# Kernel optimization log

Hardware: AMD Instinct MI355X
Metric: run time of the kernel (lower is better)

Reference implementation:

```python
import jax, jax.numpy as jnp
import numpy as np

N = 100_000      # nodes
E = 1_200_000    # edges (before self-loops)
F_IN = 128       # num_node_features
G = 256          # number of graphs in the batch
C = 10           # num_classes
NEG_SLOPE = 0.2  # PyG GATConv default


def setup_inputs() -> dict:
    key = jax.random.key(0)
    ks = jax.random.split(key, 20)
    x = jax.random.normal(ks[0], (N, F_IN), jnp.float32)
    edge_index = jax.random.randint(ks[1], (2, E), 0, N, dtype=jnp.int32)
    # sorted graph assignment covering all G graphs (no empty segments)
    batch = (jnp.arange(N, dtype=jnp.int32) * G) // N

    def lin(k, fi, fo):
        return jax.random.normal(k, (fi, fo), jnp.float32) * (1.0 / np.sqrt(fi))

    dims = [(F_IN, 16), (16, 32), (32, 64)]
    params = {}
    for i, (fi, fo) in enumerate(dims, start=1):
        params[f"W{i}"] = lin(ks[3 * i], fi, fo)
        params[f"a{i}_src"] = jax.random.normal(ks[3 * i + 1], (fo,), jnp.float32) * 0.1
        params[f"a{i}_dst"] = jax.random.normal(ks[3 * i + 2], (fo,), jnp.float32) * 0.1
        params[f"b{i}"] = jnp.zeros((fo,), jnp.float32)
    params["fc_w"] = lin(ks[15], 64, C)
    params["fc_b"] = jnp.zeros((C,), jnp.float32)
    return {"x": x, "edge_index": edge_index, "batch": batch, **params}


def _gat_layer(x, src, dst, W, a_src, a_dst, b):
    # h = Theta x; e_ij = LeakyReLU(a_src.h_j + a_dst.h_i), softmax over dst i
    h = x @ W                                     # [N, F]
    s = h @ a_src                                 # [N]
    d = h @ a_dst                                 # [N]
    logits = jax.nn.leaky_relu(s[src] + d[dst], NEG_SLOPE)   # [E+N]
    m = jax.ops.segment_max(logits, dst, num_segments=N)     # per-dst max
    ex = jnp.exp(logits - m[dst])
    denom = jax.ops.segment_sum(ex, dst, num_segments=N)
    alpha = ex / (denom[dst] + 1e-16)             # [E+N]
    out = jax.ops.segment_sum(alpha[:, None] * h[src], dst, num_segments=N)
    return out + b


def reference(x, edge_index, batch, W1, a1_src, a1_dst, b1, W2, a2_src, a2_dst, b2,
              W3, a3_src, a3_dst, b3, fc_w, fc_b):
    # add self-loops (PyG GATConv default) -> every dst segment non-empty
    loops = jnp.arange(N, dtype=edge_index.dtype)
    src = jnp.concatenate([edge_index[0], loops])
    dst = jnp.concatenate([edge_index[1], loops])

    h = jax.nn.relu(_gat_layer(x, src, dst, W1, a1_src, a1_dst, b1))
    # F.dropout(training=False) is a no-op in eval
    h = jax.nn.relu(_gat_layer(h, src, dst, W2, a2_src, a2_dst, b2))
    h = jax.nn.relu(_gat_layer(h, src, dst, W3, a3_src, a3_dst, b3))
    pooled = jax.ops.segment_max(h, batch, num_segments=G)   # global_max_pool [G, 64]
    logits = pooled @ fc_w + fc_b
    return jax.nn.log_softmax(logits, axis=1)
```

## Files before the change

kernel.cpp:

```cpp
#include <hip/hip_runtime.h>
#include <hip/hip_bf16.h>
#include <hip/hip_fp16.h>
#include <math.h>

#define NEG_SLOPE 0.2f
#define NCHUNK 1024
#define BSHIFT 9
#define BNODES 512

__device__ __forceinline__ float leaky(float x) { return x > 0.f ? x : NEG_SLOPE * x; }
__device__ __forceinline__ int usan(int v, int n) { return ((unsigned)v < (unsigned)n) ? v : 0; }

__global__ void chunk_hist(const int* __restrict__ dst, int E, int Ec, int nbuck,
                           int* __restrict__ hmatT) {
    extern __shared__ int hist[];
    int c = blockIdx.x;
    for (int b = threadIdx.x; b < nbuck; b += 256) hist[b] = 0;
    __syncthreads();
    int lo = c * Ec, hi = min(E, lo + Ec);
    for (int e = lo + threadIdx.x; e < hi; e += 256) atomicAdd(&hist[dst[e] >> BSHIFT], 1);
    __syncthreads();
    for (int b = threadIdx.x; b < nbuck; b += 256) hmatT[b * NCHUNK + c] = hist[b];
}

__global__ void mat_scan(int* __restrict__ hmatT, int* __restrict__ btot) {
    __shared__ int wsum[4];
    int b = blockIdx.x;
    int t = threadIdx.x;
    int lane = t & 63, wave = t >> 6;
    int base = b * NCHUNK + t * 4;
    int a0 = hmatT[base], a1 = hmatT[base + 1], a2 = hmatT[base + 2], a3 = hmatT[base + 3];
    int ts = a0 + a1 + a2 + a3;
    int incl = ts;
#pragma unroll
    for (int o = 1; o < 64; o <<= 1) {
        int v = __shfl_up(incl, o);
        if (lane >= o) incl += v;
    }
    if (lane == 63) wsum[wave] = incl;
    __syncthreads();
    int wadd = 0;
#pragma unroll
    for (int w = 0; w < 4; w++) if (w < wave) wadd += wsum[w];
    int excl = wadd + incl - ts;
    hmatT[base] = excl;
    hmatT[base + 1] = excl + a0;
    hmatT[base + 2] = excl + a0 + a1;
    hmatT[base + 3] = excl + a0 + a1 + a2;
    if (t == 255) btot[b] = wadd + incl;
}

__global__ void base_scan(const int* __restrict__ btot, int nbuck, int* __restrict__ bbase,
                          int* __restrict__ offs, int N, int E) {
    __shared__ int tsum[256];
    int t = threadIdx.x;
    int v = (t < nbuck) ? btot[t] : 0;
    tsum[t] = v;
    __syncthreads();
    for (int o = 1; o < 256; o <<= 1) {
        int add = (t >= o) ? tsum[t - o] : 0;
        __syncthreads();
        tsum[t] += add;
        __syncthreads();
    }
    if (t <= nbuck) bbase[t] = (t == 0) ? 0 : tsum[t - 1];
    if (t == 0) offs[N] = N + E;
}

__global__ void chunk_scatter(const int* __restrict__ src, const int* __restrict__ dst,
                              int E, int Ec, int nbuck, const int* __restrict__ hmatT,
                              const int* __restrict__ bbase, int* __restrict__ bbuf) {
    extern __shared__ int cur[];
    int c = blockIdx.x;
    for (int b = threadIdx.x; b < nbuck; b += 256) cur[b] = bbase[b] + hmatT[b * NCHUNK + c];
    __syncthreads();
    int lo = c * Ec, hi = min(E, lo + Ec);
    for (int e = lo + threadIdx.x; e < hi; e += 256) {
        int d = dst[e];
        int b = d >> BSHIFT;
        int p = atomicAdd(&cur[b], 1);
        bbuf[p] = (src[e] << BSHIFT) | (d & (BNODES - 1));
    }
}

__global__ void bucket_build(const int* __restrict__ bbase, const int* __restrict__ bbuf,
                             int N, int* __restrict__ offs, int* __restrict__ csr) {
    __shared__ int hist[BNODES];
    __shared__ int offl[BNODES];
    __shared__ int cur[BNODES];
    int b = blockIdx.x;
    int t = threadIdx.x;
    hist[t] = 0;
    __syncthreads();
    int lo = bbase[b], hi = bbase[b + 1];
    for (int j = lo + t; j < hi; j += BNODES) atomicAdd(&hist[bbuf[j] & (BNODES - 1)], 1);
    __syncthreads();
    int own = hist[t];
    for (int o = 1; o < BNODES; o <<= 1) {
        int add = (t >= o) ? hist[t - o] : 0;
        __syncthreads();
        hist[t] += add;
        __syncthreads();
    }
    int excl = hist[t] - own;
    int n = (b << BSHIFT) + t;
    int off_n = n + bbase[b] + excl;
    offl[t] = off_n;
    cur[t] = 0;
    if (n < N) {
        offs[n] = off_n;
        csr[off_n] = n;
    }
    __syncthreads();
    for (int j = lo + t; j < hi; j += BNODES) {
        int v = bbuf[j];
        int ld = v & (BNODES - 1);
        int r = atomicAdd(&cur[ld], 1);
        csr[offl[ld] + 1 + r] = v >> BSHIFT;
    }
}


template <int FIN, int FOUT>
__global__ void transform(const float* __restrict__ xin, const float* __restrict__ W,
                          const float* __restrict__ adst,
                          __half* __restrict__ h, float* __restrict__ dv, int N) {
    constexpr int TPN = FOUT / 4;
    constexpr int BN  = 256 / TPN;
    constexpr int PITCH = FIN + 4;
    __shared__ float xs[BN * PITCH];
    __shared__ float wl[FIN * FOUT];
    __shared__ float bl[FOUT];
    for (int j = threadIdx.x; j < FIN * FOUT; j += 256) wl[j] = W[j];
    if (threadIdx.x < FOUT) bl[threadIdx.x] = adst[threadIdx.x];
    int base = blockIdx.x * BN;
    constexpr int NV = BN * FIN / 4;
    const float4* xg = (const float4*)xin + (size_t)base * (FIN / 4);
    int limv = ((N - base) * FIN) >> 2;
    for (int v = threadIdx.x; v < NV; v += 256) {
        int n = v / (FIN / 4), c = v % (FIN / 4);
        float4 val = (v < limv) ? xg[v] : make_float4(0.f, 0.f, 0.f, 0.f);
        *(float4*)&xs[n * PITCH + c * 4] = val;
    }
    __syncthreads();
    int node_l = threadIdx.x / TPN;
    int fq = (threadIdx.x % TPN) * 4;
    int node = base + node_l;
    const float* xrow = &xs[node_l * PITCH];
    float4 acc = make_float4(0.f, 0.f, 0.f, 0.f);
#pragma unroll 8
    for (int k = 0; k < FIN; k++) {
        float xv = xrow[k];
        float4 w4 = *(const float4*)&wl[k * FOUT + fq];
        acc.x += xv * w4.x; acc.y += xv * w4.y; acc.z += xv * w4.z; acc.w += xv * w4.w;
    }
    if (node < N) {
        __half2* hp = (__half2*)(h + (size_t)node * FOUT + fq);
        hp[0] = __floats2half2_rn(acc.x, acc.y);
        hp[1] = __floats2half2_rn(acc.z, acc.w);
        float dp = acc.x * bl[fq] + acc.y * bl[fq + 1] + acc.z * bl[fq + 2] + acc.w * bl[fq + 3];
#pragma unroll
        for (int o = TPN / 2; o > 0; o >>= 1) dp += __shfl_xor(dp, o);
        if (fq == 0) dv[node] = dp;
    }
}


template <int FI, int FO>
__global__ void gat_trans(const __half* __restrict__ h, const float* __restrict__ asrc,
                          const float* __restrict__ dv, const int* __restrict__ offs,
                          const int* __restrict__ csr, const float* __restrict__ bias,
                          const float* __restrict__ Wn, const float* __restrict__ an_d,
                          __half* __restrict__ h2, float* __restrict__ dv2, int N) {
    constexpr int L  = FI / 8;
    constexpr int L2 = 2 * L;
    constexpr int CPL = FO / L2;
    constexpr int NPB = 256 / L2;
    __shared__ float wl[FI * FO];
    __shared__ float bl[FO];
    for (int j = threadIdx.x; j < FI * FO; j += 256) wl[j] = Wn[j];
    if (threadIdx.x < FO) bl[threadIdx.x] = an_d[threadIdx.x];
    __syncthreads();
    int lane  = threadIdx.x % L;
    int lane2 = threadIdx.x % L2;
    int wlane = threadIdx.x & 63;
    int half  = (threadIdx.x / L) & 1;
    int grpbase = wlane & ~(L2 - 1);
    int i = blockIdx.x * NPB + threadIdx.x / L2;
    if (i >= N) return;
    float asr[8];
#pragma unroll
    for (int k = 0; k < 8; k++) asr[k] = asrc[lane * 8 + k];
    int beg = offs[i], end = offs[i + 1];
    float di = dv[i];
    float acc[8];
#pragma unroll
    for (int c = 0; c < 8; c++) acc[c] = 0.f;
    float ssum = 0.f;

    int j0 = beg + 4 * half;
    int j1 = j0 + 8;
    bool vA = (j0 + 4 <= end);
    bool vB = (j1 + 4 <= end);
    int j0e = vA ? j0 : beg;
    int a0 = usan(csr[j0e], N),     a1 = usan(csr[j0e + 1], N);
    int a2 = usan(csr[j0e + 2], N), a3 = usan(csr[j0e + 3], N);
    uint4 uA0 = *((const uint4*)(h + (size_t)a0 * FI) + lane);
    uint4 uA1 = *((const uint4*)(h + (size_t)a1 * FI) + lane);
    uint4 uA2 = *((const uint4*)(h + (size_t)a2 * FI) + lane);
    uint4 uA3 = *((const uint4*)(h + (size_t)a3 * FI) + lane);
    int j1e = vB ? j1 : beg;
    int b0 = usan(csr[j1e], N),     b1 = usan(csr[j1e + 1], N);
    int b2 = usan(csr[j1e + 2], N), b3 = usan(csr[j1e + 3], N);
    while (vA) {
        int j2 = j1 + 8;
        bool vC = vB && (j2 + 4 <= end);
        uint4 uB0 = *((const uint4*)(h + (size_t)b0 * FI) + lane);
        uint4 uB1 = *((const uint4*)(h + (size_t)b1 * FI) + lane);
        uint4 uB2 = *((const uint4*)(h + (size_t)b2 * FI) + lane);
        uint4 uB3 = *((const uint4*)(h + (size_t)b3 * FI) + lane);
        int j2e = vC ? j2 : beg;
        int c0 = usan(csr[j2e], N),     c1 = usan(csr[j2e + 1], N);
        int c2 = usan(csr[j2e + 2], N), c3 = usan(csr[j2e + 3], N);
        float2 f0[4], f1[4], f2[4], f3[4];
#pragma unroll
        for (int c = 0; c < 4; c++) {
            f0[c] = __half22float2(((const __half2*)&uA0)[c]);
            f1[c] = __half22float2(((const __half2*)&uA1)[c]);
            f2[c] = __half22float2(((const __half2*)&uA2)[c]);
            f3[c] = __half22float2(((const __half2*)&uA3)[c]);
        }
        float p0 = 0.f, p1 = 0.f, p2 = 0.f, p3 = 0.f;
#pragma unroll
        for (int c = 0; c < 4; c++) {
            p0 += f0[c].x * asr[2 * c] + f0[c].y * asr[2 * c + 1];
            p1 += f1[c].x * asr[2 * c] + f1[c].y * asr[2 * c + 1];
            p2 += f2[c].x * asr[2 * c] + f2[c].y * asr[2 * c + 1];
            p3 += f3[c].x * asr[2 * c] + f3[c].y * asr[2 * c + 1];
        }
#pragma unroll
        for (int o = 1; o < L; o <<= 1) {
            p0 += __shfl_xor(p0, o); p1 += __shfl_xor(p1, o);
            p2 += __shfl_xor(p2, o); p3 += __shfl_xor(p3, o);
        }
        float w0 = __expf(leaky(p0 + di));
        float w1 = __expf(leaky(p1 + di));
        float w2 = __expf(leaky(p2 + di));
        float w3 = __expf(leaky(p3 + di));
        ssum += (w0 + w1) + (w2 + w3);
#pragma unroll
        for (int c = 0; c < 4; c++) {
            acc[2 * c]     += w0 * f0[c].x + w1 * f1[c].x + w2 * f2[c].x + w3 * f3[c].x;
            acc[2 * c + 1] += w0 * f0[c].y + w1 * f1[c].y + w2 * f2[c].y + w3 * f3[c].y;
        }
        uA0 = uB0; uA1 = uB1; uA2 = uB2; uA3 = uB3;
        b0 = c0; b1 = c1; b2 = c2; b3 = c3;
        j0 = j1; j1 = j2; vA = vB; vB = vC;
    }
    int rem = end - j0;
    if (rem > 0) {
        int o1 = rem > 1 ? 1 : 0;
        int o2 = rem > 2 ? 2 : o1;
        int t0 = usan(csr[j0], N), t1 = usan(csr[j0 + o1], N), t2 = usan(csr[j0 + o2], N);
        uint4 r0 = *((const uint4*)(h + (size_t)t0 * FI) + lane);
        uint4 r1 = *((const uint4*)(h + (size_t)t1 * FI) + lane);
        uint4 r2 = *((const uint4*)(h + (size_t)t2 * FI) + lane);
        float2 g0[4], g1[4], g2[4];
#pragma unroll
        for (int c = 0; c < 4; c++) {
            g0[c] = __half22float2(((const __half2*)&r0)[c]);
            g1[c] = __half22float2(((const __half2*)&r1)[c]);
            g2[c] = __half22float2(((const __half2*)&r2)[c]);
        }
        float q0 = 0.f, q1 = 0.f, q2 = 0.f;
#pragma unroll
        for (int c = 0; c < 4; c++) {
            q0 += g0[c].x * asr[2 * c] + g0[c].y * asr[2 * c + 1];
            q1 += g1[c].x * asr[2 * c] + g1[c].y * asr[2 * c + 1];
            q2 += g2[c].x * asr[2 * c] + g2[c].y * asr[2 * c + 1];
        }
#pragma unroll
        for (int o = 1; o < L; o <<= 1) {
            q0 += __shfl_xor(q0, o); q1 += __shfl_xor(q1, o); q2 += __shfl_xor(q2, o);
        }
        float w0t = __expf(leaky(q0 + di));
        float w1t = rem > 1 ? __expf(leaky(q1 + di)) : 0.f;
        float w2t = rem > 2 ? __expf(leaky(q2 + di)) : 0.f;
        ssum += w0t + w1t + w2t;
#pragma unroll
        for (int c = 0; c < 4; c++) {
            acc[2 * c]     += w0t * g0[c].x + w1t * g1[c].x + w2t * g2[c].x;
            acc[2 * c + 1] += w0t * g0[c].y + w1t * g1[c].y + w2t * g2[c].y;
        }
    }
#pragma unroll
    for (int c = 0; c < 8; c++) acc[c] += __shfl_xor(acc[c], L);
    ssum += __shfl_xor(ssum, L);

    float inv = 1.0f / ssum;
    float4 ba = ((const float4*)bias)[lane * 2];
    float4 bb = ((const float4*)bias)[lane * 2 + 1];
    float yv[8];
    yv[0] = fmaxf(acc[0] * inv + ba.x, 0.f);
    yv[1] = fmaxf(acc[1] * inv + ba.y, 0.f);
    yv[2] = fmaxf(acc[2] * inv + ba.z, 0.f);
    yv[3] = fmaxf(acc[3] * inv + ba.w, 0.f);
    yv[4] = fmaxf(acc[4] * inv + bb.x, 0.f);
    yv[5] = fmaxf(acc[5] * inv + bb.y, 0.f);
    yv[6] = fmaxf(acc[6] * inv + bb.z, 0.f);
    yv[7] = fmaxf(acc[7] * inv + bb.w, 0.f);
    int colbase = lane2 * CPL;
    float oacc[CPL];
#pragma unroll
    for (int c = 0; c < CPL; c++) oacc[c] = 0.f;
#pragma unroll
    for (int jj = 0; jj < L; jj++) {
        float v[8];
#pragma unroll
        for (int r = 0; r < 8; r++) v[r] = __shfl(yv[r], grpbase + jj);
#pragma unroll
        for (int r = 0; r < 8; r++) {
            const float* wrow = &wl[(jj * 8 + r) * FO + colbase];
#pragma unroll
            for (int c = 0; c < CPL; c++) oacc[c] += v[r] * wrow[c];
        }
    }
    __half2 hp[CPL / 2];
#pragma unroll
    for (int c = 0; c < CPL / 2; c++) hp[c] = __floats2half2_rn(oacc[2 * c], oacc[2 * c + 1]);
    *((uint4*)(h2 + (size_t)i * FO + colbase)) = *(uint4*)&hp[0];
    float dp = 0.f;
#pragma unroll
    for (int c = 0; c < CPL; c++) dp += oacc[c] * bl[colbase + c];
#pragma unroll
    for (int o = 1; o < L2; o <<= 1) dp += __shfl_xor(dp, o);
    if (lane2 == 0) dv2[i] = dp;
}


template <int F>
__global__ void gat_fused(const __half* __restrict__ h, const float* __restrict__ asrc,
                          const float* __restrict__ dv, const int* __restrict__ offs,
                          const int* __restrict__ csr, const float* __restrict__ bias,
                          __half* __restrict__ y, int N) {
    constexpr int L  = F / 8;
    constexpr int L2 = 2 * L;
    constexpr int NPB = 256 / L2;
    int lane  = threadIdx.x % L;
    int half  = (threadIdx.x / L) & 1;
    int i = blockIdx.x * NPB + threadIdx.x / L2;
    if (i >= N) return;
    float asr[8];
#pragma unroll
    for (int k = 0; k < 8; k++) asr[k] = asrc[lane * 8 + k];
    int beg = offs[i], end = offs[i + 1];
    float di = dv[i];
    float acc[8];
#pragma unroll
    for (int c = 0; c < 8; c++) acc[c] = 0.f;
    float ssum = 0.f;

    int j0 = beg + 4 * half;
    int j1 = j0 + 8;
    bool vA = (j0 + 4 <= end);
    bool vB = (j1 + 4 <= end);
    int j0e = vA ? j0 : beg;
    int a0 = usan(csr[j0e], N),     a1 = usan(csr[j0e + 1], N);
    int a2 = usan(csr[j0e + 2], N), a3 = usan(csr[j0e + 3], N);
    uint4 uA0 = *((const uint4*)(h + (size_t)a0 * F) + lane);
    uint4 uA1 = *((const uint4*)(h + (size_t)a1 * F) + lane);
    uint4 uA2 = *((const uint4*)(h + (size_t)a2 * F) + lane);
    uint4 uA3 = *((const uint4*)(h + (size_t)a3 * F) + lane);
    int j1e = vB ? j1 : beg;
    int b0 = usan(csr[j1e], N),     b1 = usan(csr[j1e + 1], N);
    int b2 = usan(csr[j1e + 2], N), b3 = usan(csr[j1e + 3], N);
    while (vA) {
        int j2 = j1 + 8;
        bool vC = vB && (j2 + 4 <= end);
        uint4 uB0 = *((const uint4*)(h + (size_t)b0 * F) + lane);
        uint4 uB1 = *((const uint4*)(h + (size_t)b1 * F) + lane);
        uint4 uB2 = *((const uint4*)(h + (size_t)b2 * F) + lane);
        uint4 uB3 = *((const uint4*)(h + (size_t)b3 * F) + lane);
        int j2e = vC ? j2 : beg;
        int c0 = usan(csr[j2e], N),     c1 = usan(csr[j2e + 1], N);
        int c2 = usan(csr[j2e + 2], N), c3 = usan(csr[j2e + 3], N);
        float2 f0[4], f1[4], f2[4], f3[4];
#pragma unroll
        for (int c = 0; c < 4; c++) {
            f0[c] = __half22float2(((const __half2*)&uA0)[c]);
            f1[c] = __half22float2(((const __half2*)&uA1)[c]);
            f2[c] = __half22float2(((const __half2*)&uA2)[c]);
            f3[c] = __half22float2(((const __half2*)&uA3)[c]);
        }
        float p0 = 0.f, p1 = 0.f, p2 = 0.f, p3 = 0.f;
#pragma unroll
        for (int c = 0; c < 4; c++) {
            p0 += f0[c].x * asr[2 * c] + f0[c].y * asr[2 * c + 1];
            p1 += f1[c].x * asr[2 * c] + f1[c].y * asr[2 * c + 1];
            p2 += f2[c].x * asr[2 * c] + f2[c].y * asr[2 * c + 1];
            p3 += f3[c].x * asr[2 * c] + f3[c].y * asr[2 * c + 1];
        }
#pragma unroll
        for (int o = 1; o < L; o <<= 1) {
            p0 += __shfl_xor(p0, o); p1 += __shfl_xor(p1, o);
            p2 += __shfl_xor(p2, o); p3 += __shfl_xor(p3, o);
        }
        float w0 = __expf(leaky(p0 + di));
        float w1 = __expf(leaky(p1 + di));
        float w2 = __expf(leaky(p2 + di));
        float w3 = __expf(leaky(p3 + di));
        ssum += (w0 + w1) + (w2 + w3);
#pragma unroll
        for (int c = 0; c < 4; c++) {
            acc[2 * c]     += w0 * f0[c].x + w1 * f1[c].x + w2 * f2[c].x + w3 * f3[c].x;
            acc[2 * c + 1] += w0 * f0[c].y + w1 * f1[c].y + w2 * f2[c].y + w3 * f3[c].y;
        }
        uA0 = uB0; uA1 = uB1; uA2 = uB2; uA3 = uB3;
        b0 = c0; b1 = c1; b2 = c2; b3 = c3;
        j0 = j1; j1 = j2; vA = vB; vB = vC;
    }
    int rem = end - j0;
    if (rem > 0) {
        int o1 = rem > 1 ? 1 : 0;
        int o2 = rem > 2 ? 2 : o1;
        int t0 = usan(csr[j0], N), t1 = usan(csr[j0 + o1], N), t2 = usan(csr[j0 + o2], N);
        uint4 r0 = *((const uint4*)(h + (size_t)t0 * F) + lane);
        uint4 r1 = *((const uint4*)(h + (size_t)t1 * F) + lane);
        uint4 r2 = *((const uint4*)(h + (size_t)t2 * F) + lane);
        float2 g0[4], g1[4], g2[4];
#pragma unroll
        for (int c = 0; c < 4; c++) {
            g0[c] = __half22float2(((const __half2*)&r0)[c]);
            g1[c] = __half22float2(((const __half2*)&r1)[c]);
            g2[c] = __half22float2(((const __half2*)&r2)[c]);
        }
        float q0 = 0.f, q1 = 0.f, q2 = 0.f;
#pragma unroll
        for (int c = 0; c < 4; c++) {
            q0 += g0[c].x * asr[2 * c] + g0[c].y * asr[2 * c + 1];
            q1 += g1[c].x * asr[2 * c] + g1[c].y * asr[2 * c + 1];
            q2 += g2[c].x * asr[2 * c] + g2[c].y * asr[2 * c + 1];
        }
#pragma unroll
        for (int o = 1; o < L; o <<= 1) {
            q0 += __shfl_xor(q0, o); q1 += __shfl_xor(q1, o); q2 += __shfl_xor(q2, o);
        }
        float w0t = __expf(leaky(q0 + di));
        float w1t = rem > 1 ? __expf(leaky(q1 + di)) : 0.f;
        float w2t = rem > 2 ? __expf(leaky(q2 + di)) : 0.f;
        ssum += w0t + w1t + w2t;
#pragma unroll
        for (int c = 0; c < 4; c++) {
            acc[2 * c]     += w0t * g0[c].x + w1t * g1[c].x + w2t * g2[c].x;
            acc[2 * c + 1] += w0t * g0[c].y + w1t * g1[c].y + w2t * g2[c].y;
        }
    }
#pragma unroll
    for (int c = 0; c < 8; c++) acc[c] += __shfl_xor(acc[c], L);
    ssum += __shfl_xor(ssum, L);
    if (half == 0) {
        float inv = 1.0f / ssum;
        float4 ba = ((const float4*)bias)[lane * 2];
        float4 bb = ((const float4*)bias)[lane * 2 + 1];
        __half2 o[4];
        o[0] = __floats2half2_rn(fmaxf(acc[0] * inv + ba.x, 0.f), fmaxf(acc[1] * inv + ba.y, 0.f));
        o[1] = __floats2half2_rn(fmaxf(acc[2] * inv + ba.z, 0.f), fmaxf(acc[3] * inv + ba.w, 0.f));
        o[2] = __floats2half2_rn(fmaxf(acc[4] * inv + bb.x, 0.f), fmaxf(acc[5] * inv + bb.y, 0.f));
        o[3] = __floats2half2_rn(fmaxf(acc[6] * inv + bb.z, 0.f), fmaxf(acc[7] * inv + bb.w, 0.f));
        ((uint4*)(y + (size_t)i * F))[lane] = *(uint4*)&o[0];
    }
}


__global__ void pool_head(const __half* __restrict__ y, const float* __restrict__ fcw,
                          const float* __restrict__ fcb, float* __restrict__ out,
                          int N, int G, int C) {
    __shared__ float red[256];
    __shared__ float pl[64];
    int g = blockIdx.x;
    long long gl = g;
    int start = (int)((gl * N + G - 1) / G);
    int end = (int)(((gl + 1) * N + G - 1) / G);
    int f = threadIdx.x & 63, w = threadIdx.x >> 6;
    float m = 0.f;
    for (int i = start + w; i < end; i += 4) m = fmaxf(m, __half2float(y[(size_t)i * 64 + f]));
    red[threadIdx.x] = m;
    __syncthreads();
    if (threadIdx.x < 64) {
        pl[f] = fmaxf(fmaxf(red[f], red[64 + f]), fmaxf(red[128 + f], red[192 + f]));
    }
    __syncthreads();
    if (threadIdx.x < 64) {
        int c = threadIdx.x;
        float z = -1e30f;
        if (c < C) {
            z = fcb[c];
            for (int k = 0; k < 64; k++) z += pl[k] * fcw[k * 10 + c];
        }
        float zm = z;
#pragma unroll
        for (int o = 1; o < 16; o <<= 1) zm = fmaxf(zm, __shfl_xor(zm, o));
        float e = (c < C) ? __expf(z - zm) : 0.f;
        float se = e;
#pragma unroll
        for (int o = 1; o < 16; o <<= 1) se += __shfl_xor(se, o);
        if (c < C) out[g * C + c] = z - zm - logf(se);
    }
}


extern "C" void kernel_launch(void* const* d_in, const int* in_sizes, int n_in,
                              void* d_out, int out_size, void* d_ws, size_t ws_size,
                              hipStream_t stream) {
    const float* x    = (const float*)d_in[0];
    const int*   eidx = (const int*)d_in[1];
    const float* W1 = (const float*)d_in[3];
    const float* a1s = (const float*)d_in[4];
    const float* a1d = (const float*)d_in[5];
    const float* b1 = (const float*)d_in[6];
    const float* W2 = (const float*)d_in[7];
    const float* a2s = (const float*)d_in[8];
    const float* a2d = (const float*)d_in[9];
    const float* b2 = (const float*)d_in[10];
    const float* W3 = (const float*)d_in[11];
    const float* a3s = (const float*)d_in[12];
    const float* a3d = (const float*)d_in[13];
    const float* b3 = (const float*)d_in[14];
    const float* fcw = (const float*)d_in[15];
    const float* fcb = (const float*)d_in[16];
    float* out = (float*)d_out;

    const int N = in_sizes[2];
    const int E = in_sizes[1] / 2;
    const int C = in_sizes[16];
    const int G = out_size / C;

    const int* src = eidx;
    const int* dst = eidx + E;

    size_t off = 0;
    auto alloc = [&](size_t bytes) -> void* {
        void* p = (char*)d_ws + off;
        off += (bytes + 255) & ~(size_t)255;
        return p;
    };
    int* offs   = (int*)alloc((size_t)(N + 1) * 4);
    int* csr    = (int*)alloc((size_t)(E + N) * 4 + 256);
    float* dbufA = (float*)alloc((size_t)N * 4);
    float* dbufB = (float*)alloc((size_t)N * 4);
    __half* hA = (__half*)alloc((size_t)N * 64 * 2);
    __half* hB = (__half*)alloc((size_t)N * 64 * 2);

    const int NBUCK = (N + BNODES - 1) >> BSHIFT;
    const int Ec = (E + NCHUNK - 1) / NCHUNK;
    int* hmatT = (int*)alloc((size_t)NBUCK * NCHUNK * 4);
    int* btot  = (int*)alloc((size_t)NBUCK * 4);
    int* bbase = (int*)alloc((size_t)(NBUCK + 1) * 4);
    int* bbuf  = (int*)hB;

    const size_t histBytes = (size_t)NBUCK * 4;

    chunk_hist<<<NCHUNK, 256, histBytes, stream>>>(dst, E, Ec, NBUCK, hmatT);
    mat_scan<<<NBUCK, 256, 0, stream>>>(hmatT, btot);
    base_scan<<<1, 256, 0, stream>>>(btot, NBUCK, bbase, offs, N, E);
    chunk_scatter<<<NCHUNK, 256, histBytes, stream>>>(src, dst, E, Ec, NBUCK, hmatT, bbase, bbuf);
    bucket_build<<<NBUCK, BNODES, 0, stream>>>(bbase, bbuf, N, offs, csr);

    transform<128, 16><<<(N + 63) / 64, 256, 0, stream>>>(x, W1, a1d, hA, dbufA, N);
    gat_trans<16, 32><<<(N + 63) / 64, 256, 0, stream>>>(hA, a1s, dbufA, offs, csr, b1,
                                                         W2, a2d, hB, dbufB, N);
    gat_trans<32, 64><<<(N + 31) / 32, 256, 0, stream>>>(hB, a2s, dbufB, offs, csr, b2,
                                                         W3, a3d, hA, dbufA, N);
    gat_fused<64><<<(N + 15) / 16, 256, 0, stream>>>(hA, a3s, dbufA, offs, csr, b3, hB, N);

    pool_head<<<G, 256, 0, stream>>>(hB, fcw, fcb, out, N, G, C);
}
```

Measured before the change: 274.5 us.

## Fuse global max pool into last GAT layer via atomicMax; shrink CSR buckets

The last GAT layer now max-pools its ReLU outputs straight into a per-graph pooled buffer. It does this with atomicMax on the float bits, going through a shared-memory reduction when a block covers a single graph. This removes the write and reread of the final N×64 half activations and leaves a tiny head kernel. The CSR bucket size also drops from 512 to 256 nodes, and the block-level scans in base_scan and bucket_build switch to wave-shuffle scans with 512 threads. The risk is that NBUCK (about 391) must stay at or below 512 threads, and the pooled buffer must be zeroed each call, which base_scan now does.

```diff
diff --git a/kernel.cpp b/kernel.cpp
--- a/kernel.cpp
+++ b/kernel.cpp
@@ -5,8 +5,8 @@
 
 #define NEG_SLOPE 0.2f
 #define NCHUNK 1024
-#define BSHIFT 9
-#define BNODES 512
+#define BSHIFT 8
+#define BNODES 256
 
 __device__ __forceinline__ float leaky(float x) { return x > 0.f ? x : NEG_SLOPE * x; }
 __device__ __forceinline__ int usan(int v, int n) { return ((unsigned)v < (unsigned)n) ? v : 0; }
@@ -51,20 +51,27 @@
 }
 
 __global__ void base_scan(const int* __restrict__ btot, int nbuck, int* __restrict__ bbase,
-                          int* __restrict__ offs, int N, int E) {
-    __shared__ int tsum[256];
+                          int* __restrict__ offs, int N, int E, float* __restrict__ pooled,
+                          int PG) {
+    __shared__ int wsum[8];
     int t = threadIdx.x;
+    int lane = t & 63, wave = t >> 6;
     int v = (t < nbuck) ? btot[t] : 0;
-    tsum[t] = v;
-    __syncthreads();
-    for (int o = 1; o < 256; o <<= 1) {
-        int add = (t >= o) ? tsum[t - o] : 0;
-        __syncthreads();
-        tsum[t] += add;
-        __syncthreads();
-    }
-    if (t <= nbuck) bbase[t] = (t == 0) ? 0 : tsum[t - 1];
+    int incl = v;
+#pragma unroll
+    for (int o = 1; o < 64; o <<= 1) {
+        int s = __shfl_up(incl, o);
+        if (lane >= o) incl += s;
+    }
+    if (lane == 63) wsum[wave] = incl;
+    __syncthreads();
+    int wadd = 0;
+#pragma unroll
+    for (int w = 0; w < 8; w++) if (w < wave) wadd += wsum[w];
+    incl += wadd;
+    if (t <= nbuck) bbase[t] = incl - v;
     if (t == 0) offs[N] = N + E;
+    for (int k = t; k < PG; k += 512) pooled[k] = 0.f;
 }
 
 __global__ void chunk_scatter(const int* __restrict__ src, const int* __restrict__ dst,
@@ -88,21 +95,28 @@
     __shared__ int hist[BNODES];
     __shared__ int offl[BNODES];
     __shared__ int cur[BNODES];
+    __shared__ int wsum[4];
     int b = blockIdx.x;
     int t = threadIdx.x;
+    int lane = t & 63, wave = t >> 6;
     hist[t] = 0;
     __syncthreads();
     int lo = bbase[b], hi = bbase[b + 1];
     for (int j = lo + t; j < hi; j += BNODES) atomicAdd(&hist[bbuf[j] & (BNODES - 1)], 1);
     __syncthreads();
     int own = hist[t];
-    for (int o = 1; o < BNODES; o <<= 1) {
-        int add = (t >= o) ? hist[t - o] : 0;
-        __syncthreads();
-        hist[t] += add;
-        __syncthreads();
-    }
-    int excl = hist[t] - own;
+    int incl = own;
+#pragma unroll
+    for (int o = 1; o < 64; o <<= 1) {
+        int s = __shfl_up(incl, o);
+        if (lane >= o) incl += s;
+    }
+    if (lane == 63) wsum[wave] = incl;
+    __syncthreads();
+    int wadd = 0;
+#pragma unroll
+    for (int w = 0; w < 4; w++) if (w < wave) wadd += wsum[w];
+    int excl = wadd + incl - own;
     int n = (b << BSHIFT) + t;
     int off_n = n + bbase[b] + excl;
     offl[t] = off_n;
@@ -342,170 +356,184 @@
 __global__ void gat_fused(const __half* __restrict__ h, const float* __restrict__ asrc,
                           const float* __restrict__ dv, const int* __restrict__ offs,
                           const int* __restrict__ csr, const float* __restrict__ bias,
-                          __half* __restrict__ y, int N) {
+                          float* __restrict__ pooled, int Gn, int N) {
     constexpr int L  = F / 8;
     constexpr int L2 = 2 * L;
     constexpr int NPB = 256 / L2;
+    __shared__ unsigned pl[64];
     int lane  = threadIdx.x % L;
     int half  = (threadIdx.x / L) & 1;
     int i = blockIdx.x * NPB + threadIdx.x / L2;
-    if (i >= N) return;
-    float asr[8];
-#pragma unroll
-    for (int k = 0; k < 8; k++) asr[k] = asrc[lane * 8 + k];
-    int beg = offs[i], end = offs[i + 1];
-    float di = dv[i];
-    float acc[8];
-#pragma unroll
-    for (int c = 0; c < 8; c++) acc[c] = 0.f;
-    float ssum = 0.f;
-
-    int j0 = beg + 4 * half;
-    int j1 = j0 + 8;
-    bool vA = (j0 + 4 <= end);
-    bool vB = (j1 + 4 <= end);
-    int j0e = vA ? j0 : beg;
-    int a0 = usan(csr[j0e], N),     a1 = usan(csr[j0e + 1], N);
-    int a2 = usan(csr[j0e + 2], N), a3 = usan(csr[j0e + 3], N);
-    uint4 uA0 = *((const uint4*)(h + (size_t)a0 * F) + lane);
-    uint4 uA1 = *((const uint4*)(h + (size_t)a1 * F) + lane);
-    uint4 uA2 = *((const uint4*)(h + (size_t)a2 * F) + lane);
-    uint4 uA3 = *((const uint4*)(h + (size_t)a3 * F) + lane);
-    int j1e = vB ? j1 : beg;
-    int b0 = usan(csr[j1e], N),     b1 = usan(csr[j1e + 1], N);
-    int b2 = usan(csr[j1e + 2], N), b3 = usan(csr[j1e + 3], N);
-    while (vA) {
-        int j2 = j1 + 8;
-        bool vC = vB && (j2 + 4 <= end);
-        uint4 uB0 = *((const uint4*)(h + (size_t)b0 * F) + lane);
-        uint4 uB1 = *((const uint4*)(h + (size_t)b1 * F) + lane);
-        uint4 uB2 = *((const uint4*)(h + (size_t)b2 * F) + lane);
-        uint4 uB3 = *((const uint4*)(h + (size_t)b3 * F) + lane);
-        int j2e = vC ? j2 : beg;
-        int c0 = usan(csr[j2e], N),     c1 = usan(csr[j2e + 1], N);
-        int c2 = usan(csr[j2e + 2], N), c3 = usan(csr[j2e + 3], N);
-        float2 f0[4], f1[4], f2[4], f3[4];
-#pragma unroll
-        for (int c = 0; c < 4; c++) {
-            f0[c] = __half22float2(((const __half2*)&uA0)[c]);
-            f1[c] = __half22float2(((const __half2*)&uA1)[c]);
-            f2[c] = __half22float2(((const __half2*)&uA2)[c]);
-            f3[c] = __half22float2(((const __half2*)&uA3)[c]);
-        }
-        float p0 = 0.f, p1 = 0.f, p2 = 0.f, p3 = 0.f;
-#pragma unroll
-        for (int c = 0; c < 4; c++) {
-            p0 += f0[c].x * asr[2 * c] + f0[c].y * asr[2 * c + 1];
-            p1 += f1[c].x * asr[2 * c] + f1[c].y * asr[2 * c + 1];
-            p2 += f2[c].x * asr[2 * c] + f2[c].y * asr[2 * c + 1];
-            p3 += f3[c].x * asr[2 * c] + f3[c].y * asr[2 * c + 1];
-        }
-#pragma unroll
-        for (int o = 1; o < L; o <<= 1) {
-            p0 += __shfl_xor(p0, o); p1 += __shfl_xor(p1, o);
-            p2 += __shfl_xor(p2, o); p3 += __shfl_xor(p3, o);
-        }
-        float w0 = __expf(leaky(p0 + di));
-        float w1 = __expf(leaky(p1 + di));
-        float w2 = __expf(leaky(p2 + di));
-        float w3 = __expf(leaky(p3 + di));
-        ssum += (w0 + w1) + (w2 + w3);
-#pragma unroll
-        for (int c = 0; c < 4; c++) {
-            acc[2 * c]     += w0 * f0[c].x + w1 * f1[c].x + w2 * f2[c].x + w3 * f3[c].x;
-            acc[2 * c + 1] += w0 * f0[c].y + w1 * f1[c].y + w2 * f2[c].y + w3 * f3[c].y;
-        }
-        uA0 = uB0; uA1 = uB1; uA2 = uB2; uA3 = uB3;
-        b0 = c0; b1 = c1; b2 = c2; b3 = c3;
-        j0 = j1; j1 = j2; vA = vB; vB = vC;
-    }
-    int rem = end - j0;
-    if (rem > 0) {
-        int o1 = rem > 1 ? 1 : 0;
-        int o2 = rem > 2 ? 2 : o1;
-        int t0 = usan(csr[j0], N), t1 = usan(csr[j0 + o1], N), t2 = usan(csr[j0 + o2], N);
-        uint4 r0 = *((const uint4*)(h + (size_t)t0 * F) + lane);
-        uint4 r1 = *((const uint4*)(h + (size_t)t1 * F) + lane);
-        uint4 r2 = *((const uint4*)(h + (size_t)t2 * F) + lane);
-        float2 g0[4], g1[4], g2[4];
-#pragma unroll
-        for (int c = 0; c < 4; c++) {
-            g0[c] = __half22float2(((const __half2*)&r0)[c]);
-            g1[c] = __half22float2(((const __half2*)&r1)[c]);
-            g2[c] = __half22float2(((const __half2*)&r2)[c]);
-        }
-        float q0 = 0.f, q1 = 0.f, q2 = 0.f;
-#pragma unroll
-        for (int c = 0; c < 4; c++) {
-            q0 += g0[c].x * asr[2 * c] + g0[c].y * asr[2 * c + 1];
-            q1 += g1[c].x * asr[2 * c] + g1[c].y * asr[2 * c + 1];
-            q2 += g2[c].x * asr[2 * c] + g2[c].y * asr[2 * c + 1];
-        }
-#pragma unroll
-        for (int o = 1; o < L; o <<= 1) {
-            q0 += __shfl_xor(q0, o); q1 += __shfl_xor(q1, o); q2 += __shfl_xor(q2, o);
-        }
-        float w0t = __expf(leaky(q0 + di));
-        float w1t = rem > 1 ? __expf(leaky(q1 + di)) : 0.f;
-        float w2t = rem > 2 ? __expf(leaky(q2 + di)) : 0.f;
-        ssum += w0t + w1t + w2t;
-#pragma unroll
-        for (int c = 0; c < 4; c++) {
-            acc[2 * c]     += w0t * g0[c].x + w1t * g1[c].x + w2t * g2[c].x;
-            acc[2 * c + 1] += w0t * g0[c].y + w1t * g1[c].y + w2t * g2[c].y;
-        }
-    }
-#pragma unroll
-    for (int c = 0; c < 8; c++) acc[c] += __shfl_xor(acc[c], L);
-    ssum += __shfl_xor(ssum, L);
-    if (half == 0) {
+    bool active = (i < N);
+    float yf[8];
+#pragma unroll
+    for (int c = 0; c < 8; c++) yf[c] = 0.f;
+    if (active) {
+        float asr[8];
+#pragma unroll
+        for (int k = 0; k < 8; k++) asr[k] = asrc[lane * 8 + k];
+        int beg = offs[i], end = offs[i + 1];
+        float di = dv[i];
+        float acc[8];
+#pragma unroll
+        for (int c = 0; c < 8; c++) acc[c] = 0.f;
+        float ssum = 0.f;
+
+        int j0 = beg + 4 * half;
+        int j1 = j0 + 8;
+        bool vA = (j0 + 4 <= end);
+        bool vB = (j1 + 4 <= end);
+        int j0e = vA ? j0 : beg;
+        int a0 = usan(csr[j0e], N),     a1 = usan(csr[j0e + 1], N);
+        int a2 = usan(csr[j0e + 2], N), a3 = usan(csr[j0e + 3], N);
+        uint4 uA0 = *((const uint4*)(h + (size_t)a0 * F) + lane);
+        uint4 uA1 = *((const uint4*)(h + (size_t)a1 * F) + lane);
+        uint4 uA2 = *((const uint4*)(h + (size_t)a2 * F) + lane);
+        uint4 uA3 = *((const uint4*)(h + (size_t)a3 * F) + lane);
+        int j1e = vB ? j1 : beg;
+        int b0 = usan(csr[j1e], N),     b1 = usan(csr[j1e + 1], N);
+        int b2 = usan(csr[j1e + 2], N), b3 = usan(csr[j1e + 3], N);
+        while (vA) {
+            int j2 = j1 + 8;
+            bool vC = vB && (j2 + 4 <= end);
+            uint4 uB0 = *((const uint4*)(h + (size_t)b0 * F) + lane);
+            uint4 uB1 = *((const uint4*)(h + (size_t)b1 * F) + lane);
+            uint4 uB2 = *((const uint4*)(h + (size_t)b2 * F) + lane);
+            uint4 uB3 = *((const uint4*)(h + (size_t)b3 * F) + lane);
+            int j2e = vC ? j2 : beg;
+            int c0 = usan(csr[j2e], N),     c1 = usan(csr[j2e + 1], N);
+            int c2 = usan(csr[j2e + 2], N), c3 = usan(csr[j2e + 3], N);
+            float2 f0[4], f1[4], f2[4], f3[4];
+#pragma unroll
+            for (int c = 0; c < 4; c++) {
+                f0[c] = __half22float2(((const __half2*)&uA0)[c]);
+                f1[c] = __half22float2(((const __half2*)&uA1)[c]);
+                f2[c] = __half22float2(((const __half2*)&uA2)[c]);
+                f3[c] = __half22float2(((const __half2*)&uA3)[c]);
+            }
+            float p0 = 0.f, p1 = 0.f, p2 = 0.f, p3 = 0.f;
+#pragma unroll
+            for (int c = 0; c < 4; c++) {
+                p0 += f0[c].x * asr[2 * c] + f0[c].y * asr[2 * c + 1];
+                p1 += f1[c].x * asr[2 * c] + f1[c].y * asr[2 * c + 1];
+                p2 += f2[c].x * asr[2 * c] + f2[c].y * asr[2 * c + 1];
+                p3 += f3[c].x * asr[2 * c] + f3[c].y * asr[2 * c + 1];
+            }
+#pragma unroll
+            for (int o = 1; o < L; o <<= 1) {
+                p0 += __shfl_xor(p0, o); p1 += __shfl_xor(p1, o);
+                p2 += __shfl_xor(p2, o); p3 += __shfl_xor(p3, o);
+            }
+            float w0 = __expf(leaky(p0 + di));
+            float w1 = __expf(leaky(p1 + di));
+            float w2 = __expf(leaky(p2 + di));
+            float w3 = __expf(leaky(p3 + di));
+            ssum += (w0 + w1) + (w2 + w3);
+#pragma unroll
+            for (int c = 0; c < 4; c++) {
+                acc[2 * c]     += w0 * f0[c].x + w1 * f1[c].x + w2 * f2[c].x + w3 * f3[c].x;
+                acc[2 * c + 1] += w0 * f0[c].y + w1 * f1[c].y + w2 * f2[c].y + w3 * f3[c].y;
+            }
+            uA0 = uB0; uA1 = uB1; uA2 = uB2; uA3 = uB3;
+            b0 = c0; b1 = c1; b2 = c2; b3 = c3;
+            j0 = j1; j1 = j2; vA = vB; vB = vC;
+        }
+        int rem = end - j0;
+        if (rem > 0) {
+            int o1 = rem > 1 ? 1 : 0;
+            int o2 = rem > 2 ? 2 : o1;
+            int t0 = usan(csr[j0], N), t1 = usan(csr[j0 + o1], N), t2 = usan(csr[j0 + o2], N);
+            uint4 r0 = *((const uint4*)(h + (size_t)t0 * F) + lane);
+            uint4 r1 = *((const uint4*)(h + (size_t)t1 * F) + lane);
+            uint4 r2 = *((const uint4*)(h + (size_t)t2 * F) + lane);
+            float2 g0[4], g1[4], g2[4];
+#pragma unroll
+            for (int c = 0; c < 4; c++) {
+                g0[c] = __half22float2(((const __half2*)&r0)[c]);
+                g1[c] = __half22float2(((const __half2*)&r1)[c]);
+                g2[c] = __half22float2(((const __half2*)&r2)[c]);
+            }
+            float q0 = 0.f, q1 = 0.f, q2 = 0.f;
+#pragma unroll
+            for (int c = 0; c < 4; c++) {
+                q0 += g0[c].x * asr[2 * c] + g0[c].y * asr[2 * c + 1];
+                q1 += g1[c].x * asr[2 * c] + g1[c].y * asr[2 * c + 1];
+                q2 += g2[c].x * asr[2 * c] + g2[c].y * asr[2 * c + 1];
+            }
+#pragma unroll
+            for (int o = 1; o < L; o <<= 1) {
+                q0 += __shfl_xor(q0, o); q1 += __shfl_xor(q1, o); q2 += __shfl_xor(q2, o);
+            }
+            float w0t = __expf(leaky(q0 + di));
+            float w1t = rem > 1 ? __expf(leaky(q1 + di)) : 0.f;
+            float w2t = rem > 2 ? __expf(leaky(q2 + di)) : 0.f;
+            ssum += w0t + w1t + w2t;
+#pragma unroll
+            for (int c = 0; c < 4; c++) {
+                acc[2 * c]     += w0t * g0[c].x + w1t * g1[c].x + w2t * g2[c].x;
+                acc[2 * c + 1] += w0t * g0[c].y + w1t * g1[c].y + w2t * g2[c].y;
+            }
+        }
+#pragma unroll
+        for (int c = 0; c < 8; c++) acc[c] += __shfl_xor(acc[c], L);
+        ssum += __shfl_xor(ssum, L);
         float inv = 1.0f / ssum;
         float4 ba = ((const float4*)bias)[lane * 2];
         float4 bb = ((const float4*)bias)[lane * 2 + 1];
-        __half2 o[4];
-        o[0] = __floats2half2_rn(fmaxf(acc[0] * inv + ba.x, 0.f), fmaxf(acc[1] * inv + ba.y, 0.f));
-        o[1] = __floats2half2_rn(fmaxf(acc[2] * inv + ba.z, 0.f), fmaxf(acc[3] * inv + ba.w, 0.f));
-        o[2] = __floats2half2_rn(fmaxf(acc[4] * inv + bb.x, 0.f), fmaxf(acc[5] * inv + bb.y, 0.f));
-        o[3] = __floats2half2_rn(fmaxf(acc[6] * inv + bb.z, 0.f), fmaxf(acc[7] * inv + bb.w, 0.f));
-        ((uint4*)(y + (size_t)i * F))[lane] = *(uint4*)&o[0];
-    }
-}
-
-
-__global__ void pool_head(const __half* __restrict__ y, const float* __restrict__ fcw,
-                          const float* __restrict__ fcb, float* __restrict__ out,
-                          int N, int G, int C) {
-    __shared__ float red[256];
+        yf[0] = fmaxf(acc[0] * inv + ba.x, 0.f);
+        yf[1] = fmaxf(acc[1] * inv + ba.y, 0.f);
+        yf[2] = fmaxf(acc[2] * inv + ba.z, 0.f);
+        yf[3] = fmaxf(acc[3] * inv + ba.w, 0.f);
+        yf[4] = fmaxf(acc[4] * inv + bb.x, 0.f);
+        yf[5] = fmaxf(acc[5] * inv + bb.y, 0.f);
+        yf[6] = fmaxf(acc[6] * inv + bb.z, 0.f);
+        yf[7] = fmaxf(acc[7] * inv + bb.w, 0.f);
+    }
+    int i0 = blockIdx.x * NPB;
+    int ilast = min(i0 + NPB, N) - 1;
+    int gfirst = (int)(((long long)i0 * Gn) / N);
+    int glast  = (int)(((long long)ilast * Gn) / N);
+    if (threadIdx.x < 64) pl[threadIdx.x] = 0u;
+    __syncthreads();
+    if (active && half == 0) {
+        if (gfirst == glast) {
+#pragma unroll
+            for (int k = 0; k < 8; k++) atomicMax(&pl[lane * 8 + k], __float_as_uint(yf[k]));
+        } else {
+            int g = (int)(((long long)i * Gn) / N);
+#pragma unroll
+            for (int k = 0; k < 8; k++)
+                atomicMax((unsigned*)&pooled[(size_t)g * 64 + lane * 8 + k], __float_as_uint(yf[k]));
+        }
+    }
+    __syncthreads();
+    if (gfirst == glast && threadIdx.x < 64) {
+        unsigned v = pl[threadIdx.x];
+        if (v) atomicMax((unsigned*)&pooled[(size_t)gfirst * 64 + threadIdx.x], v);
+    }
+}
+
+
+__global__ void head(const float* __restrict__ pooled, const float* __restrict__ fcw,
+                     const float* __restrict__ fcb, float* __restrict__ out, int C) {
     __shared__ float pl[64];
     int g = blockIdx.x;
-    long long gl = g;
-    int start = (int)((gl * N + G - 1) / G);
-    int end = (int)(((gl + 1) * N + G - 1) / G);
-    int f = threadIdx.x & 63, w = threadIdx.x >> 6;
-    float m = 0.f;
-    for (int i = start + w; i < end; i += 4) m = fmaxf(m, __half2float(y[(size_t)i * 64 + f]));
-    red[threadIdx.x] = m;
-    __syncthreads();
-    if (threadIdx.x < 64) {
-        pl[f] = fmaxf(fmaxf(red[f], red[64 + f]), fmaxf(red[128 + f], red[192 + f]));
-    }
-    __syncthreads();
-    if (threadIdx.x < 64) {
-        int c = threadIdx.x;
-        float z = -1e30f;
-        if (c < C) {
-            z = fcb[c];
-            for (int k = 0; k < 64; k++) z += pl[k] * fcw[k * 10 + c];
-        }
-        float zm = z;
-#pragma unroll
-        for (int o = 1; o < 16; o <<= 1) zm = fmaxf(zm, __shfl_xor(zm, o));
-        float e = (c < C) ? __expf(z - zm) : 0.f;
-        float se = e;
-#pragma unroll
-        for (int o = 1; o < 16; o <<= 1) se += __shfl_xor(se, o);
-        if (c < C) out[g * C + c] = z - zm - logf(se);
-    }
+    int c = threadIdx.x;
+    pl[c] = pooled[(size_t)g * 64 + c];
+    __syncthreads();
+    float z = -1e30f;
+    if (c < C) {
+        z = fcb[c];
+        for (int k = 0; k < 64; k++) z += pl[k] * fcw[k * 10 + c];
+    }
+    float zm = z;
+#pragma unroll
+    for (int o = 1; o < 16; o <<= 1) zm = fmaxf(zm, __shfl_xor(zm, o));
+    float e = (c < C) ? __expf(z - zm) : 0.f;
+    float se = e;
+#pragma unroll
+    for (int o = 1; o < 16; o <<= 1) se += __shfl_xor(se, o);
+    if (c < C) out[g * C + c] = z - zm - logf(se);
 }
 
 
@@ -548,6 +576,7 @@
     int* csr    = (int*)alloc((size_t)(E + N) * 4 + 256);
     float* dbufA = (float*)alloc((size_t)N * 4);
     float* dbufB = (float*)alloc((size_t)N * 4);
+    float* pooled = (float*)alloc((size_t)G * 64 * 4);
     __half* hA = (__half*)alloc((size_t)N * 64 * 2);
     __half* hB = (__half*)alloc((size_t)N * 64 * 2);
 
@@ -562,7 +591,7 @@
 
     chunk_hist<<<NCHUNK, 256, histBytes, stream>>>(dst, E, Ec, NBUCK, hmatT);
     mat_scan<<<NBUCK, 256, 0, stream>>>(hmatT, btot);
-    base_scan<<<1, 256, 0, stream>>>(btot, NBUCK, bbase, offs, N, E);
+    base_scan<<<1, 512, 0, stream>>>(btot, NBUCK, bbase, offs, N, E, pooled, G * 64);
     chunk_scatter<<<NCHUNK, 256, histBytes, stream>>>(src, dst, E, Ec, NBUCK, hmatT, bbase, bbuf);
     bucket_build<<<NBUCK, BNODES, 0, stream>>>(bbase, bbuf, N, offs, csr);
 
@@ -571,7 +600,7 @@
                                                          W2, a2d, hB, dbufB, N);
     gat_trans<32, 64><<<(N + 31) / 32, 256, 0, stream>>>(hB, a2s, dbufB, offs, csr, b2,
                                                          W3, a3d, hA, dbufA, N);
-    gat_fused<64><<<(N + 15) / 16, 256, 0, stream>>>(hA, a3s, dbufA, offs, csr, b3, hB, N);
-
-    pool_head<<<G, 256, 0, stream>>>(hB, fcw, fcb, out, N, G, C);
-}
+    gat_fused<64><<<(N + 15) / 16, 256, 0, stream>>>(hA, a3s, dbufA, offs, csr, b3, pooled, G, N);
+
+    head<<<G, 64, 0, stream>>>(pooled, fcw, fcb, out, C);
+}
```

Result: slower. 284.5 us (+3.6%).
